# Performance work log

Hardware: AMD Instinct MI355X
Metric: run time of the kernel (lower is better)

Reference implementation:

```python
import jax, jax.numpy as jnp
import numpy as np

S, B, DIM = 1024, 4, 768
N_EXPERTS = 8
# hidden_dim = 256 * ceil(int(2*4*dim/3)/256) = 2048 for dim=768
HID = 2048


def setup_inputs() -> dict:
    key = jax.random.key(0)
    ks = jax.random.split(key, 6)
    scale = 0.02
    return {
        "hidden_states": jax.random.normal(ks[0], (S, B, DIM), dtype=jnp.float32),
        "router_w": jax.random.normal(ks[1], (DIM, N_EXPERTS), dtype=jnp.float32) * scale,
        "router_b": jnp.zeros((N_EXPERTS,), dtype=jnp.float32),
        "w1": jax.random.normal(ks[2], (N_EXPERTS, DIM, HID), dtype=jnp.float32) * scale,
        "w2": jax.random.normal(ks[3], (N_EXPERTS, DIM, HID), dtype=jnp.float32) * scale,
        "w3": jax.random.normal(ks[4], (N_EXPERTS, HID, DIM), dtype=jnp.float32) * scale,
    }


def reference(hidden_states, router_w, router_b, w1, w2, w3):
    s, b, h = hidden_states.shape
    # top-1 router
    route = jax.nn.softmax(hidden_states @ router_w + router_b, axis=2)  # [s,b,E]
    max_prob = jnp.max(route, axis=2).reshape(-1, 1)   # [T,1]
    max_ind = jnp.argmax(route, axis=2).reshape(-1)    # [T]
    x = hidden_states.reshape(-1, h)                   # [T,d]

    out = jnp.zeros_like(x)
    # fixed small loop over experts; masked dispatch (tokens not routed to e
    # are zeroed so they contribute nothing)
    for e in range(N_EXPERTS):
        mask = (max_ind == e)[:, None]                 # [T,1]
        xe = jnp.where(mask, x, 0.0)
        oe = (jax.nn.silu(xe @ w1[e]) * (xe @ w2[e])) @ w3[e]
        out = out + jnp.where(mask, oe, 0.0)

    # original stores expert outputs in a bf16 buffer before the prob combine
    out = out.astype(jnp.bfloat16) * max_prob          # bf16 * f32 -> f32
    return out.reshape(s, b, h)
```

## Files before the change

### kernel.cpp

```cpp
#include <hip/hip_runtime.h>


#define T_TOK 4096
#define DIM   768
#define HID   2048
#define NE    8
#define ECAP  1024

#define KB1 24
#define NB1 128
#define KB2 64
#define NB2 48
#define MBC 64

typedef _Float16 f16x8 __attribute__((ext_vector_type(8)));
typedef float    f32x4 __attribute__((ext_vector_type(4)));

__device__ __forceinline__ float bf16_rne(float v) {
    unsigned u = __float_as_uint(v);
    unsigned r = (u + 0x7fffu + ((u >> 16) & 1u)) & 0xffff0000u;
    return __uint_as_float(r);
}

__global__ void moe_init_kernel(int* __restrict__ counts) {
    if (threadIdx.x < NE) counts[threadIdx.x] = 0;
}

__global__ __launch_bounds__(256) void moe_convert_kernel(
    const float* __restrict__ w1, const float* __restrict__ w2,
    const float* __restrict__ w3, _Float16* __restrict__ w1s,
    _Float16* __restrict__ w2s, _Float16* __restrict__ w3s)
{
    const int bid = blockIdx.x;
    const float* src; _Float16* dst; int N, KBc, ngrp, kgrp;
    if (bid < 1536) {
        const int e = bid / 192, tile = bid % 192;
        src = w1 + (size_t)e * DIM * HID; dst = w1s + (size_t)e * NB1 * KB1 * 512;
        N = HID; KBc = KB1; ngrp = tile & 15; kgrp = tile >> 4;
    } else if (bid < 3072) {
        const int r = bid - 1536, e = r / 192, tile = r % 192;
        src = w2 + (size_t)e * DIM * HID; dst = w2s + (size_t)e * NB1 * KB1 * 512;
        N = HID; KBc = KB1; ngrp = tile & 15; kgrp = tile >> 4;
    } else {
        const int r = bid - 3072, e = r / 192, tile = r % 192;
        src = w3 + (size_t)e * HID * DIM; dst = w3s + (size_t)e * NB2 * KB2 * 512;
        N = DIM; KBc = KB2; ngrp = tile % 6; kgrp = tile / 6;
    }

    __shared__ float Lt[64 * 130];
    const int t  = threadIdx.x;
    const int c4 = (t & 31) * 4;
    const int r0 = (t >> 5) * 8;
    const float* p = src + (size_t)(kgrp * 64 + r0) * N + ngrp * 128 + c4;
    float4 v[8];
#pragma unroll
    for (int j = 0; j < 8; ++j) v[j] = *(const float4*)(p + (size_t)j * N);
#pragma unroll
    for (int j = 0; j < 8; ++j) {
        float* row = &Lt[(r0 + j) * 130 + c4];
        *(float2*)(row)     = make_float2(v[j].x, v[j].y);
        *(float2*)(row + 2) = make_float2(v[j].z, v[j].w);
    }
    __syncthreads();

    const int l = t & 63, w = t >> 6;
    const int fr = l & 15, fq = l >> 4;
#pragma unroll
    for (int i = 0; i < 4; ++i) {
        const int cell = w * 4 + i;
        const int kbl = cell >> 3, nbl = cell & 7;
        f16x8 h;
#pragma unroll
        for (int j = 0; j < 8; ++j)
            h[j] = (_Float16)Lt[(kbl * 32 + fq * 8 + j) * 130 + nbl * 16 + fr];
        const int nb = ngrp * 8 + nbl, kb = kgrp * 2 + kbl;
        *(f16x8*)(dst + ((size_t)nb * KBc + kb) * 512 + l * 8) = h;
    }
}

__global__ __launch_bounds__(256) void moe_router_kernel(
    const float* __restrict__ X, const float* __restrict__ rw,
    const float* __restrict__ rb, float* __restrict__ probs,
    int* __restrict__ counts, int* __restrict__ lists)
{
    const int t    = blockIdx.x * 4 + (threadIdx.x >> 6);
    const int lane = threadIdx.x & 63;
    const float* x = X + (size_t)t * DIM;

    float xv[12];
#pragma unroll
    for (int j = 0; j < 12; ++j) xv[j] = x[lane + j * 64];

    double lg[NE];
#pragma unroll
    for (int e = 0; e < NE; ++e) {
        double s = 0.0;
#pragma unroll
        for (int j = 0; j < 12; ++j)
            s += (double)xv[j] * (double)rw[(lane + j * 64) * NE + e];
#pragma unroll
        for (int off = 32; off >= 1; off >>= 1) s += __shfl_xor(s, off, 64);
        lg[e] = s + (double)rb[e];
    }

    if (lane == 0) {
        double m = lg[0]; int mi = 0;
#pragma unroll
        for (int e = 1; e < NE; ++e)
            if (lg[e] > m) { m = lg[e]; mi = e; }
        float sum = 0.f;
#pragma unroll
        for (int e = 0; e < NE; ++e) sum += expf((float)(lg[e] - m));
        probs[t] = 1.0f / sum;
        int pos = atomicAdd(&counts[mi], 1);
        lists[mi * T_TOK + pos] = t;
    }
}

__global__ __launch_bounds__(256) void moe_gather_kernel(
    const float* __restrict__ X, const int* __restrict__ lists,
    const int* __restrict__ counts, _Float16* __restrict__ Ag)
{
    const int e = blockIdx.z;
    int cnt = counts[e]; if (cnt > ECAP) cnt = ECAP;
    const int mgrp = blockIdx.y;
    if (mgrp * 64 >= ((cnt + 63) & ~63)) return;
    const int t = threadIdx.x, w = t >> 6, l = t & 63;
    const int mb = mgrp * 4 + w;
    const int m  = mb * 16 + (l & 15);
    const bool valid = (m < cnt);
    const int tok = valid ? lists[e * T_TOK + m] : 0;
    const float* xr = X + (size_t)tok * DIM + (l >> 4) * 8;
#pragma unroll
    for (int i = 0; i < 4; ++i) {
        const int kb = blockIdx.x * 4 + i;
        float4 a = make_float4(0.f, 0.f, 0.f, 0.f), b = a;
        if (valid) {
            a = *(const float4*)(xr + kb * 32);
            b = *(const float4*)(xr + kb * 32 + 4);
        }
        f16x8 h;
        h[0] = (_Float16)a.x; h[1] = (_Float16)a.y; h[2] = (_Float16)a.z; h[3] = (_Float16)a.w;
        h[4] = (_Float16)b.x; h[5] = (_Float16)b.y; h[6] = (_Float16)b.z; h[7] = (_Float16)b.w;
        *(f16x8*)(Ag + ((size_t)(e * MBC + mb) * KB1 + kb) * 512 + l * 8) = h;
    }
}

__global__ __launch_bounds__(256, 3) void moe_gemm1_kernel(
    const _Float16* __restrict__ Ag, const _Float16* __restrict__ w1s,
    const _Float16* __restrict__ w2s, const int* __restrict__ counts,
    _Float16* __restrict__ Hs)
{
    const int e = blockIdx.z;
    int cnt = counts[e]; if (cnt > ECAP) cnt = ECAP;
    const int by = blockIdx.y, bx = blockIdx.x;
    if (by * 128 >= cnt) return;
    const int t = threadIdx.x, w = t >> 6, l = t & 63;
    const int wm = w & 1, wn = w >> 1;

    __shared__ _Float16 Ls[2][16 * 512];
    __shared__ _Float16 Ep[4][64 * 40];

    const int c0s = w * 4;
    const _Float16* gsrc[4];
#pragma unroll
    for (int i = 0; i < 4; ++i) {
        const int c = c0s + i;
        if (c < 8)
            gsrc[i] = Ag  + ((size_t)((e * MBC + by * 8 + c) * KB1)) * 512;
        else if (c < 12)
            gsrc[i] = w1s + ((size_t)((e * NB1 + bx * 4 + (c - 8)) * KB1)) * 512;
        else
            gsrc[i] = w2s + ((size_t)((e * NB1 + bx * 4 + (c - 12)) * KB1)) * 512;
        gsrc[i] += (size_t)l * 8;
    }

    f32x4 acc1[4][2], acc2[4][2];
    const f32x4 zero = {0.f, 0.f, 0.f, 0.f};
#pragma unroll
    for (int i = 0; i < 4; ++i)
#pragma unroll
        for (int j = 0; j < 2; ++j) { acc1[i][j] = zero; acc2[i][j] = zero; }

    f16x8 st[4];
    auto G = [&](int kb) {
#pragma unroll
        for (int i = 0; i < 4; ++i)
            st[i] = *(const f16x8*)(gsrc[i] + (size_t)kb * 512);
    };

    G(0);
    for (int kb = 0; kb < KB1; ++kb) {
        _Float16* Lb = &Ls[kb & 1][0];
#pragma unroll
        for (int i = 0; i < 4; ++i)
            *(f16x8*)(Lb + (c0s + i) * 512 + l * 8) = st[i];
        __syncthreads();
        if (kb + 1 < KB1) G(kb + 1);

        f16x8 a[4], p[2], q[2];
#pragma unroll
        for (int i = 0; i < 4; ++i)
            a[i] = *(const f16x8*)(Lb + (wm * 4 + i) * 512 + l * 8);
#pragma unroll
        for (int j = 0; j < 2; ++j) {
            p[j] = *(const f16x8*)(Lb + (8  + wn * 2 + j) * 512 + l * 8);
            q[j] = *(const f16x8*)(Lb + (12 + wn * 2 + j) * 512 + l * 8);
        }
#pragma unroll
        for (int i = 0; i < 4; ++i)
#pragma unroll
            for (int j = 0; j < 2; ++j) {
                acc1[i][j] = __builtin_amdgcn_mfma_f32_16x16x32_f16(a[i], p[j], acc1[i][j], 0, 0, 0);
                acc2[i][j] = __builtin_amdgcn_mfma_f32_16x16x32_f16(a[i], q[j], acc2[i][j], 0, 0, 0);
            }
    }

    const int fq = l >> 4, fr = l & 15;
#pragma unroll
    for (int i = 0; i < 4; ++i)
#pragma unroll
        for (int j = 0; j < 2; ++j)
#pragma unroll
            for (int r = 0; r < 4; ++r) {
                const float h1 = acc1[i][j][r], h2 = acc2[i][j][r];
                const float s  = h1 / (1.f + __expf(-h1)) * h2;
                Ep[w][(i * 16 + fq * 4 + r) * 40 + j * 16 + fr] = (_Float16)s;
            }
    __syncthreads();
    const int kbH = bx * 2 + wn;
#pragma unroll
    for (int i = 0; i < 4; ++i) {
        f16x8 v = *(const f16x8*)&Ep[w][(i * 16 + fr) * 40 + fq * 8];
        *(f16x8*)(Hs + ((size_t)((e * MBC + by * 8 + wm * 4 + i) * KB2 + kbH)) * 512 + l * 8) = v;
    }
}

__global__ __launch_bounds__(256, 3) void moe_gemm2_kernel(
    const _Float16* __restrict__ Hs, const _Float16* __restrict__ w3s,
    const int* __restrict__ lists, const int* __restrict__ counts,
    const float* __restrict__ probs, float* __restrict__ out)
{
    const int e = blockIdx.z;
    int cnt = counts[e]; if (cnt > ECAP) cnt = ECAP;
    const int by = blockIdx.y, bx = blockIdx.x;
    if (by * 64 >= cnt) return;
    const int t = threadIdx.x, w = t >> 6, l = t & 63;

    __shared__ _Float16 Ls[2][24 * 512];

    const int c0s = w * 3;
    const _Float16* gsrc[3];
#pragma unroll
    for (int i = 0; i < 3; ++i) {
        const int c = c0s + i;
        if (c < 4)
            gsrc[i] = Hs  + ((size_t)((e * MBC + by * 4 + c) * KB2)) * 512;
        else
            gsrc[i] = w3s + ((size_t)((e * NB2 + bx * 8 + (c - 4)) * KB2)) * 512;
        gsrc[i] += (size_t)l * 8;
    }

    f32x4 acc[4][2];
    const f32x4 zero = {0.f, 0.f, 0.f, 0.f};
#pragma unroll
    for (int i = 0; i < 4; ++i) { acc[i][0] = zero; acc[i][1] = zero; }

    f16x8 st[6];
    auto G = [&](int kb0) {
#pragma unroll
        for (int u = 0; u < 2; ++u)
#pragma unroll
            for (int i = 0; i < 3; ++i)
                st[u * 3 + i] = *(const f16x8*)(gsrc[i] + (size_t)(kb0 + u) * 512);
    };

    G(0);
    for (int s = 0; s < KB2 / 2; ++s) {
        _Float16* Lb = &Ls[s & 1][0];
#pragma unroll
        for (int u = 0; u < 2; ++u)
#pragma unroll
            for (int i = 0; i < 3; ++i)
                *(f16x8*)(Lb + (u * 12 + c0s + i) * 512 + l * 8) = st[u * 3 + i];
        __syncthreads();
        if (s + 1 < KB2 / 2) G(2 * (s + 1));

#pragma unroll
        for (int u = 0; u < 2; ++u) {
            f16x8 a[4], b[2];
#pragma unroll
            for (int i = 0; i < 4; ++i)
                a[i] = *(const f16x8*)(Lb + (u * 12 + i) * 512 + l * 8);
#pragma unroll
            for (int j = 0; j < 2; ++j)
                b[j] = *(const f16x8*)(Lb + (u * 12 + 4 + w * 2 + j) * 512 + l * 8);
#pragma unroll
            for (int i = 0; i < 4; ++i)
#pragma unroll
                for (int j = 0; j < 2; ++j)
                    acc[i][j] = __builtin_amdgcn_mfma_f32_16x16x32_f16(a[i], b[j], acc[i][j], 0, 0, 0);
        }
    }

    const int* list = lists + e * T_TOK;
    const int fq = l >> 4, fr = l & 15;
    const int c0 = bx * 128 + w * 32;
#pragma unroll
    for (int i = 0; i < 4; ++i)
#pragma unroll
        for (int r = 0; r < 4; ++r) {
            const int m = by * 64 + i * 16 + fq * 4 + r;
            if (m < cnt) {
                const int tok = list[m];
                const float pb = probs[tok];
                float* orow = out + (size_t)tok * DIM + c0 + fr;
                orow[0]  = bf16_rne(acc[i][0][r]) * pb;
                orow[16] = bf16_rne(acc[i][1][r]) * pb;
            }
        }
}

extern "C" void kernel_launch(void* const* d_in, const int* in_sizes, int n_in,
                              void* d_out, int out_size, void* d_ws, size_t ws_size,
                              hipStream_t stream) {
    const float* X  = (const float*)d_in[0];
    const float* rw = (const float*)d_in[1];
    const float* rb = (const float*)d_in[2];
    const float* w1 = (const float*)d_in[3];
    const float* w2 = (const float*)d_in[4];
    const float* w3 = (const float*)d_in[5];
    float* out = (float*)d_out;

    char* ws = (char*)d_ws;
    int*      counts = (int*)(ws + 0);
    int*      lists  = (int*)(ws + 256);
    float*    probs  = (float*)(ws + 131328);
    const size_t WSZ = 25165824;
    _Float16* w1s = (_Float16*)(ws + 147712);
    _Float16* w2s = (_Float16*)(ws + 147712 + WSZ);
    _Float16* w3s = (_Float16*)(ws + 147712 + 2 * WSZ);
    _Float16* Ag  = (_Float16*)(ws + 147712 + 3 * WSZ);
    _Float16* Hs  = (_Float16*)(ws + 147712 + 3 * WSZ + 12582912);

    hipLaunchKernelGGL(moe_init_kernel, dim3(1), dim3(64), 0, stream, counts);
    hipLaunchKernelGGL(moe_convert_kernel, dim3(4608), dim3(256), 0, stream,
                       w1, w2, w3, w1s, w2s, w3s);
    hipLaunchKernelGGL(moe_router_kernel, dim3(T_TOK / 4), dim3(256), 0, stream,
                       X, rw, rb, probs, counts, lists);
    hipLaunchKernelGGL(moe_gather_kernel, dim3(6, 16, 8), dim3(256), 0, stream,
                       X, lists, counts, Ag);
    hipLaunchKernelGGL(moe_gemm1_kernel, dim3(32, 8, 8), dim3(256), 0, stream,
                       Ag, w1s, w2s, counts, Hs);
    hipLaunchKernelGGL(moe_gemm2_kernel, dim3(6, 16, 8), dim3(256), 0, stream,
                       Hs, w3s, lists, counts, probs, out);
}
```

Baseline: 323.3 us.

## Enlarge GEMM tiles to 128x128 per block and split weight conversion kernels

GEMM1 now computes a 128x128 output tile of both gate and up projections per block (4x4 MFMA fragments per wave), halving the grid along N. GEMM2 goes from 64-row to 128-row tiles with a 2x2 wave layout. Both raise arithmetic intensity per shared-memory load, which should cut redundant global and LDS traffic. In exchange they use more registers and LDS and target occupancy 2 instead of 3. The single fused fp16 weight-conversion kernel is also split into three per-matrix launches that share a helper.

Result: slower. 344.1 us (+6.4%).

```diff
diff --git a/kernel.cpp b/kernel.cpp
--- a/kernel.cpp
+++ b/kernel.cpp
@@ -26,28 +26,10 @@
     if (threadIdx.x < NE) counts[threadIdx.x] = 0;
 }
 
-__global__ __launch_bounds__(256) void moe_convert_kernel(
-    const float* __restrict__ w1, const float* __restrict__ w2,
-    const float* __restrict__ w3, _Float16* __restrict__ w1s,
-    _Float16* __restrict__ w2s, _Float16* __restrict__ w3s)
-{
-    const int bid = blockIdx.x;
-    const float* src; _Float16* dst; int N, KBc, ngrp, kgrp;
-    if (bid < 1536) {
-        const int e = bid / 192, tile = bid % 192;
-        src = w1 + (size_t)e * DIM * HID; dst = w1s + (size_t)e * NB1 * KB1 * 512;
-        N = HID; KBc = KB1; ngrp = tile & 15; kgrp = tile >> 4;
-    } else if (bid < 3072) {
-        const int r = bid - 1536, e = r / 192, tile = r % 192;
-        src = w2 + (size_t)e * DIM * HID; dst = w2s + (size_t)e * NB1 * KB1 * 512;
-        N = HID; KBc = KB1; ngrp = tile & 15; kgrp = tile >> 4;
-    } else {
-        const int r = bid - 3072, e = r / 192, tile = r % 192;
-        src = w3 + (size_t)e * HID * DIM; dst = w3s + (size_t)e * NB2 * KB2 * 512;
-        N = DIM; KBc = KB2; ngrp = tile % 6; kgrp = tile / 6;
-    }
-
-    __shared__ float Lt[64 * 130];
+__device__ __forceinline__ void convert_tile(
+    const float* __restrict__ src, _Float16* __restrict__ dst,
+    float* Lt, int N, int KBc, int ngrp, int kgrp)
+{
     const int t  = threadIdx.x;
     const int c4 = (t & 31) * 4;
     const int r0 = (t >> 5) * 8;
@@ -76,6 +58,33 @@
         const int nb = ngrp * 8 + nbl, kb = kgrp * 2 + kbl;
         *(f16x8*)(dst + ((size_t)nb * KBc + kb) * 512 + l * 8) = h;
     }
+}
+
+__global__ __launch_bounds__(256) void moe_convert_w1_kernel(
+    const float* __restrict__ w1, _Float16* __restrict__ w1s)
+{
+    __shared__ float Lt[64 * 130];
+    const int e = blockIdx.x / 192, tile = blockIdx.x % 192;
+    convert_tile(w1 + (size_t)e * DIM * HID, w1s + (size_t)e * NB1 * KB1 * 512,
+                 Lt, HID, KB1, tile & 15, tile >> 4);
+}
+
+__global__ __launch_bounds__(256) void moe_convert_w2_kernel(
+    const float* __restrict__ w2, _Float16* __restrict__ w2s)
+{
+    __shared__ float Lt[64 * 130];
+    const int e = blockIdx.x / 192, tile = blockIdx.x % 192;
+    convert_tile(w2 + (size_t)e * DIM * HID, w2s + (size_t)e * NB1 * KB1 * 512,
+                 Lt, HID, KB1, tile & 15, tile >> 4);
+}
+
+__global__ __launch_bounds__(256) void moe_convert_w3_kernel(
+    const float* __restrict__ w3, _Float16* __restrict__ w3s)
+{
+    __shared__ float Lt[64 * 130];
+    const int e = blockIdx.x / 192, tile = blockIdx.x % 192;
+    convert_tile(w3 + (size_t)e * HID * DIM, w3s + (size_t)e * NB2 * KB2 * 512,
+                 Lt, DIM, KB2, tile % 6, tile / 6);
 }
 
 __global__ __launch_bounds__(256) void moe_router_kernel(
@@ -146,7 +155,7 @@
     }
 }
 
-__global__ __launch_bounds__(256, 3) void moe_gemm1_kernel(
+__global__ __launch_bounds__(256, 2) void moe_gemm1_kernel(
     const _Float16* __restrict__ Ag, const _Float16* __restrict__ w1s,
     const _Float16* __restrict__ w2s, const int* __restrict__ counts,
     _Float16* __restrict__ Hs)
@@ -158,8 +167,100 @@
     const int t = threadIdx.x, w = t >> 6, l = t & 63;
     const int wm = w & 1, wn = w >> 1;
 
-    __shared__ _Float16 Ls[2][16 * 512];
-    __shared__ _Float16 Ep[4][64 * 40];
+    __shared__ _Float16 Ls[2][24 * 512];
+
+    const int c0s = w * 6;
+    const _Float16* gsrc[6];
+#pragma unroll
+    for (int i = 0; i < 6; ++i) {
+        const int c = c0s + i;
+        if (c < 8)
+            gsrc[i] = Ag  + ((size_t)((e * MBC + by * 8 + c) * KB1)) * 512;
+        else if (c < 16)
+            gsrc[i] = w1s + ((size_t)((e * NB1 + bx * 8 + (c - 8)) * KB1)) * 512;
+        else
+            gsrc[i] = w2s + ((size_t)((e * NB1 + bx * 8 + (c - 16)) * KB1)) * 512;
+        gsrc[i] += (size_t)l * 8;
+    }
+
+    f32x4 acc1[4][4], acc2[4][4];
+    const f32x4 zero = {0.f, 0.f, 0.f, 0.f};
+#pragma unroll
+    for (int i = 0; i < 4; ++i)
+#pragma unroll
+        for (int j = 0; j < 4; ++j) { acc1[i][j] = zero; acc2[i][j] = zero; }
+
+    f16x8 st[6];
+    auto G = [&](int kb) {
+#pragma unroll
+        for (int i = 0; i < 6; ++i)
+            st[i] = *(const f16x8*)(gsrc[i] + (size_t)kb * 512);
+    };
+
+    G(0);
+    for (int kb = 0; kb < KB1; ++kb) {
+        _Float16* Lb = &Ls[kb & 1][0];
+#pragma unroll
+        for (int i = 0; i < 6; ++i)
+            *(f16x8*)(Lb + (c0s + i) * 512 + l * 8) = st[i];
+        __syncthreads();
+        if (kb + 1 < KB1) G(kb + 1);
+
+        f16x8 a[4], p[4], q[4];
+#pragma unroll
+        for (int i = 0; i < 4; ++i)
+            a[i] = *(const f16x8*)(Lb + (wm * 4 + i) * 512 + l * 8);
+#pragma unroll
+        for (int j = 0; j < 4; ++j) {
+            p[j] = *(const f16x8*)(Lb + (8  + wn * 4 + j) * 512 + l * 8);
+            q[j] = *(const f16x8*)(Lb + (16 + wn * 4 + j) * 512 + l * 8);
+        }
+#pragma unroll
+        for (int i = 0; i < 4; ++i)
+#pragma unroll
+            for (int j = 0; j < 4; ++j) {
+                acc1[i][j] = __builtin_amdgcn_mfma_f32_16x16x32_f16(a[i], p[j], acc1[i][j], 0, 0, 0);
+                acc2[i][j] = __builtin_amdgcn_mfma_f32_16x16x32_f16(a[i], q[j], acc2[i][j], 0, 0, 0);
+            }
+    }
+
+    __syncthreads();
+    _Float16* Ep = &Ls[0][0] + (size_t)w * (64 * 72);
+    const int fq = l >> 4, fr = l & 15;
+#pragma unroll
+    for (int i = 0; i < 4; ++i)
+#pragma unroll
+        for (int j = 0; j < 4; ++j)
+#pragma unroll
+            for (int r = 0; r < 4; ++r) {
+                const float h1 = acc1[i][j][r], h2 = acc2[i][j][r];
+                const float s  = h1 / (1.f + __expf(-h1)) * h2;
+                Ep[(i * 16 + fq * 4 + r) * 72 + j * 16 + fr] = (_Float16)s;
+            }
+    __syncthreads();
+#pragma unroll
+    for (int i = 0; i < 4; ++i)
+#pragma unroll
+        for (int h = 0; h < 2; ++h) {
+            f16x8 v = *(const f16x8*)&Ep[(i * 16 + fr) * 72 + h * 32 + fq * 8];
+            const int kbH = bx * 4 + wn * 2 + h;
+            *(f16x8*)(Hs + ((size_t)((e * MBC + by * 8 + wm * 4 + i) * KB2 + kbH)) * 512 + l * 8) = v;
+        }
+}
+
+__global__ __launch_bounds__(256, 2) void moe_gemm2_kernel(
+    const _Float16* __restrict__ Hs, const _Float16* __restrict__ w3s,
+    const int* __restrict__ lists, const int* __restrict__ counts,
+    const float* __restrict__ probs, float* __restrict__ out)
+{
+    const int e = blockIdx.z;
+    int cnt = counts[e]; if (cnt > ECAP) cnt = ECAP;
+    const int by = blockIdx.y, bx = blockIdx.x;
+    if (by * 128 >= cnt) return;
+    const int t = threadIdx.x, w = t >> 6, l = t & 63;
+    const int wm = w & 1, wn = w >> 1;
+
+    __shared__ _Float16 Ls[2][32 * 512];
 
     const int c0s = w * 4;
     const _Float16* gsrc[4];
@@ -167,112 +268,26 @@
     for (int i = 0; i < 4; ++i) {
         const int c = c0s + i;
         if (c < 8)
-            gsrc[i] = Ag  + ((size_t)((e * MBC + by * 8 + c) * KB1)) * 512;
-        else if (c < 12)
-            gsrc[i] = w1s + ((size_t)((e * NB1 + bx * 4 + (c - 8)) * KB1)) * 512;
+            gsrc[i] = Hs  + ((size_t)((e * MBC + by * 8 + c) * KB2)) * 512;
         else
-            gsrc[i] = w2s + ((size_t)((e * NB1 + bx * 4 + (c - 12)) * KB1)) * 512;
+            gsrc[i] = w3s + ((size_t)((e * NB2 + bx * 8 + (c - 8)) * KB2)) * 512;
         gsrc[i] += (size_t)l * 8;
     }
 
-    f32x4 acc1[4][2], acc2[4][2];
+    f32x4 acc[4][4];
     const f32x4 zero = {0.f, 0.f, 0.f, 0.f};
 #pragma unroll
     for (int i = 0; i < 4; ++i)
 #pragma unroll
-        for (int j = 0; j < 2; ++j) { acc1[i][j] = zero; acc2[i][j] = zero; }
-
-    f16x8 st[4];
-    auto G = [&](int kb) {
-#pragma unroll
-        for (int i = 0; i < 4; ++i)
-            st[i] = *(const f16x8*)(gsrc[i] + (size_t)kb * 512);
-    };
-
-    G(0);
-    for (int kb = 0; kb < KB1; ++kb) {
-        _Float16* Lb = &Ls[kb & 1][0];
-#pragma unroll
-        for (int i = 0; i < 4; ++i)
-            *(f16x8*)(Lb + (c0s + i) * 512 + l * 8) = st[i];
-        __syncthreads();
-        if (kb + 1 < KB1) G(kb + 1);
-
-        f16x8 a[4], p[2], q[2];
-#pragma unroll
-        for (int i = 0; i < 4; ++i)
-            a[i] = *(const f16x8*)(Lb + (wm * 4 + i) * 512 + l * 8);
-#pragma unroll
-        for (int j = 0; j < 2; ++j) {
-            p[j] = *(const f16x8*)(Lb + (8  + wn * 2 + j) * 512 + l * 8);
-            q[j] = *(const f16x8*)(Lb + (12 + wn * 2 + j) * 512 + l * 8);
-        }
-#pragma unroll
-        for (int i = 0; i < 4; ++i)
-#pragma unroll
-            for (int j = 0; j < 2; ++j) {
-                acc1[i][j] = __builtin_amdgcn_mfma_f32_16x16x32_f16(a[i], p[j], acc1[i][j], 0, 0, 0);
-                acc2[i][j] = __builtin_amdgcn_mfma_f32_16x16x32_f16(a[i], q[j], acc2[i][j], 0, 0, 0);
-            }
-    }
-
-    const int fq = l >> 4, fr = l & 15;
-#pragma unroll
-    for (int i = 0; i < 4; ++i)
-#pragma unroll
-        for (int j = 0; j < 2; ++j)
-#pragma unroll
-            for (int r = 0; r < 4; ++r) {
-                const float h1 = acc1[i][j][r], h2 = acc2[i][j][r];
-                const float s  = h1 / (1.f + __expf(-h1)) * h2;
-                Ep[w][(i * 16 + fq * 4 + r) * 40 + j * 16 + fr] = (_Float16)s;
-            }
-    __syncthreads();
-    const int kbH = bx * 2 + wn;
-#pragma unroll
-    for (int i = 0; i < 4; ++i) {
-        f16x8 v = *(const f16x8*)&Ep[w][(i * 16 + fr) * 40 + fq * 8];
-        *(f16x8*)(Hs + ((size_t)((e * MBC + by * 8 + wm * 4 + i) * KB2 + kbH)) * 512 + l * 8) = v;
-    }
-}
-
-__global__ __launch_bounds__(256, 3) void moe_gemm2_kernel(
-    const _Float16* __restrict__ Hs, const _Float16* __restrict__ w3s,
-    const int* __restrict__ lists, const int* __restrict__ counts,
-    const float* __restrict__ probs, float* __restrict__ out)
-{
-    const int e = blockIdx.z;
-    int cnt = counts[e]; if (cnt > ECAP) cnt = ECAP;
-    const int by = blockIdx.y, bx = blockIdx.x;
-    if (by * 64 >= cnt) return;
-    const int t = threadIdx.x, w = t >> 6, l = t & 63;
-
-    __shared__ _Float16 Ls[2][24 * 512];
-
-    const int c0s = w * 3;
-    const _Float16* gsrc[3];
-#pragma unroll
-    for (int i = 0; i < 3; ++i) {
-        const int c = c0s + i;
-        if (c < 4)
-            gsrc[i] = Hs  + ((size_t)((e * MBC + by * 4 + c) * KB2)) * 512;
-        else
-            gsrc[i] = w3s + ((size_t)((e * NB2 + bx * 8 + (c - 4)) * KB2)) * 512;
-        gsrc[i] += (size_t)l * 8;
-    }
-
-    f32x4 acc[4][2];
-    const f32x4 zero = {0.f, 0.f, 0.f, 0.f};
-#pragma unroll
-    for (int i = 0; i < 4; ++i) { acc[i][0] = zero; acc[i][1] = zero; }
-
-    f16x8 st[6];
+        for (int j = 0; j < 4; ++j) acc[i][j] = zero;
+
+    f16x8 st[8];
     auto G = [&](int kb0) {
 #pragma unroll
         for (int u = 0; u < 2; ++u)
 #pragma unroll
-            for (int i = 0; i < 3; ++i)
-                st[u * 3 + i] = *(const f16x8*)(gsrc[i] + (size_t)(kb0 + u) * 512);
+            for (int i = 0; i < 4; ++i)
+                st[u * 4 + i] = *(const f16x8*)(gsrc[i] + (size_t)(kb0 + u) * 512);
     };
 
     G(0);
@@ -281,42 +296,43 @@
 #pragma unroll
         for (int u = 0; u < 2; ++u)
 #pragma unroll
-            for (int i = 0; i < 3; ++i)
-                *(f16x8*)(Lb + (u * 12 + c0s + i) * 512 + l * 8) = st[u * 3 + i];
+            for (int i = 0; i < 4; ++i)
+                *(f16x8*)(Lb + (u * 16 + c0s + i) * 512 + l * 8) = st[u * 4 + i];
         __syncthreads();
         if (s + 1 < KB2 / 2) G(2 * (s + 1));
 
 #pragma unroll
         for (int u = 0; u < 2; ++u) {
-            f16x8 a[4], b[2];
+            f16x8 a[4], b[4];
 #pragma unroll
             for (int i = 0; i < 4; ++i)
-                a[i] = *(const f16x8*)(Lb + (u * 12 + i) * 512 + l * 8);
-#pragma unroll
-            for (int j = 0; j < 2; ++j)
-                b[j] = *(const f16x8*)(Lb + (u * 12 + 4 + w * 2 + j) * 512 + l * 8);
+                a[i] = *(const f16x8*)(Lb + (u * 16 + wm * 4 + i) * 512 + l * 8);
+#pragma unroll
+            for (int j = 0; j < 4; ++j)
+                b[j] = *(const f16x8*)(Lb + (u * 16 + 8 + wn * 4 + j) * 512 + l * 8);
 #pragma unroll
             for (int i = 0; i < 4; ++i)
 #pragma unroll
-                for (int j = 0; j < 2; ++j)
+                for (int j = 0; j < 4; ++j)
                     acc[i][j] = __builtin_amdgcn_mfma_f32_16x16x32_f16(a[i], b[j], acc[i][j], 0, 0, 0);
         }
     }
 
     const int* list = lists + e * T_TOK;
     const int fq = l >> 4, fr = l & 15;
-    const int c0 = bx * 128 + w * 32;
+    const int c0 = bx * 128 + wn * 64;
 #pragma unroll
     for (int i = 0; i < 4; ++i)
 #pragma unroll
         for (int r = 0; r < 4; ++r) {
-            const int m = by * 64 + i * 16 + fq * 4 + r;
+            const int m = by * 128 + wm * 64 + i * 16 + fq * 4 + r;
             if (m < cnt) {
                 const int tok = list[m];
                 const float pb = probs[tok];
                 float* orow = out + (size_t)tok * DIM + c0 + fr;
-                orow[0]  = bf16_rne(acc[i][0][r]) * pb;
-                orow[16] = bf16_rne(acc[i][1][r]) * pb;
+#pragma unroll
+                for (int j = 0; j < 4; ++j)
+                    orow[j * 16] = bf16_rne(acc[i][j][r]) * pb;
             }
         }
 }
@@ -344,14 +360,15 @@
     _Float16* Hs  = (_Float16*)(ws + 147712 + 3 * WSZ + 12582912);
 
     hipLaunchKernelGGL(moe_init_kernel, dim3(1), dim3(64), 0, stream, counts);
-    hipLaunchKernelGGL(moe_convert_kernel, dim3(4608), dim3(256), 0, stream,
-                       w1, w2, w3, w1s, w2s, w3s);
+    hipLaunchKernelGGL(moe_convert_w1_kernel, dim3(1536), dim3(256), 0, stream, w1, w1s);
+    hipLaunchKernelGGL(moe_convert_w2_kernel, dim3(1536), dim3(256), 0, stream, w2, w2s);
+    hipLaunchKernelGGL(moe_convert_w3_kernel, dim3(1536), dim3(256), 0, stream, w3, w3s);
     hipLaunchKernelGGL(moe_router_kernel, dim3(T_TOK / 4), dim3(256), 0, stream,
                        X, rw, rb, probs, counts, lists);
     hipLaunchKernelGGL(moe_gather_kernel, dim3(6, 16, 8), dim3(256), 0, stream,
                        X, lists, counts, Ag);
-    hipLaunchKernelGGL(moe_gemm1_kernel, dim3(32, 8, 8), dim3(256), 0, stream,
+    hipLaunchKernelGGL(moe_gemm1_kernel, dim3(16, 8, 8), dim3(256), 0, stream,
                        Ag, w1s, w2s, counts, Hs);
-    hipLaunchKernelGGL(moe_gemm2_kernel, dim3(6, 16, 8), dim3(256), 0, stream,
+    hipLaunchKernelGGL(moe_gemm2_kernel, dim3(6, 8, 8), dim3(256), 0, stream,
                        Hs, w3s, lists, counts, probs, out);
 }
```
